# Kernel optimization log

Measured on AMD Instinct MI355X. Metric: run time of the kernel, lower is better.

## Reference

```python
import jax, jax.numpy as jnp
import numpy as np
import math

B, S, E = 4, 2048, 1024


def setup_inputs() -> dict:
    key = jax.random.key(0)
    ks = jax.random.split(key, 9)
    x = jax.random.normal(ks[0], (B, S, E), dtype=jnp.float32)
    # causal boolean mask, broadcast over batch: True = keep
    mask = jnp.broadcast_to(jnp.tril(jnp.ones((S, S), dtype=bool)), (B, S, S))
    sc = 1.0 / math.sqrt(E)
    Wq = jax.random.normal(ks[1], (E, E), dtype=jnp.float32) * sc
    bq = jnp.zeros((E,), dtype=jnp.float32)
    Wk = jax.random.normal(ks[2], (E, E), dtype=jnp.float32) * sc
    bk = jnp.zeros((E,), dtype=jnp.float32)
    Wv = jax.random.normal(ks[3], (E, E), dtype=jnp.float32) * sc
    bv = jnp.zeros((E,), dtype=jnp.float32)
    gamma = jnp.ones((E,), dtype=jnp.float32)
    beta = jnp.zeros((E,), dtype=jnp.float32)
    return {"x": x, "mask": mask, "Wq": Wq, "bq": bq, "Wk": Wk, "bk": bk,
            "Wv": Wv, "bv": bv, "gamma": gamma, "beta": beta}


def reference(x, mask, Wq, bq, Wk, bk, Wv, bv, gamma, beta):
    E_ = x.shape[-1]
    q = jnp.einsum('bse,fe->bsf', x, Wq) + bq
    k = jnp.einsum('bse,fe->bsf', x, Wk) + bk
    v = jnp.einsum('bse,fe->bsf', x, Wv) + bv
    scores = jnp.einsum('bqe,bke->bqk', q, k) / jnp.sqrt(jnp.float32(E_))
    scores = jnp.where(mask, scores, -jnp.inf)
    probs = jax.nn.softmax(scores, axis=-1)
    attn = jnp.einsum('bqk,bke->bqe', probs, v)
    y = attn + x
    # LayerNorm over last dim, eps matches torch default 1e-5
    mu = jnp.mean(y, axis=-1, keepdims=True)
    var = jnp.mean(jnp.square(y - mu), axis=-1, keepdims=True)
    return (y - mu) / jnp.sqrt(var + 1e-5) * gamma + beta
```

## Files before the change

### kernel.cpp

```cpp
#include <hip/hip_runtime.h>
#include <hip/hip_bf16.h>
#include <stdint.h>

#define B_ 4
#define S_ 2048
#define E_ 1024
#define BS_ (B_*S_)

using bf16x8 = __attribute__((ext_vector_type(8))) __bf16;
using f32x4  = __attribute__((ext_vector_type(4))) float;

__device__ __forceinline__ unsigned short f2bf(float f) {
  unsigned int u = __float_as_uint(f);
  u += 0x7fffu + ((u >> 16) & 1u);
  return (unsigned short)(u >> 16);
}
__device__ __forceinline__ float bf2f(unsigned short h) {
  return __uint_as_float(((unsigned int)h) << 16);
}

__device__ __forceinline__ void gld16(const unsigned short* g, unsigned short* l) {
  __builtin_amdgcn_global_load_lds((__attribute__((address_space(1))) void*)(void*)g,
                                   (__attribute__((address_space(3))) void*)l, 16, 0, 0);
}

__global__ __launch_bounds__(256) void conv_f32_bf16(const float* __restrict__ in,
                                                     unsigned short* __restrict__ out,
                                                     int n4) {
  int i = blockIdx.x * 256 + threadIdx.x;
  if (i >= n4) return;
  const float4 v = ((const float4*)in)[i];
  ushort4 o;
  o.x = f2bf(v.x); o.y = f2bf(v.y); o.z = f2bf(v.z); o.w = f2bf(v.w);
  ((ushort4*)out)[i] = o;
}

__global__ __launch_bounds__(256) void concat_bias(const float* __restrict__ a,
                                                   const float* __restrict__ b,
                                                   const float* __restrict__ c,
                                                   float* __restrict__ o) {
  int i = blockIdx.x * 256 + threadIdx.x;
  if (i >= 3 * E_) return;
  o[i] = (i < E_) ? a[i] : (i < 2 * E_ ? b[i - E_] : c[i - 2 * E_]);
}

template<int EPI>
__global__ __launch_bounds__(256, 2) void gemm_bt(
    const unsigned short* __restrict__ A, const unsigned short* __restrict__ Bm,
    float* __restrict__ Cf, unsigned short* __restrict__ Cb,
    const float* __restrict__ bias,
    int K, int lda, int ldb, int ldc,
    long sA, long sB, long sC, float scale, int causal)
{
  constexpr int BM = 128, BN = 128, BK = 64;
  __shared__ __align__(16) unsigned short As[BM * BK];
  __shared__ __align__(16) unsigned short Bs[BN * BK];
  const int bz = blockIdx.z;
  A  += sA * bz;
  Bm += sB * bz;
  const int m0 = blockIdx.y * BM, n0 = blockIdx.x * BN;
  if (EPI == 1 && causal && n0 >= m0 + BM) return;
  const int kend = (EPI == 2 && causal) ? min(K, m0 + BM) : K;
  const int t = threadIdx.x;
  const int lane = t & 63, wave = t >> 6;
  const int wr = wave >> 1, wc = wave & 1;
  const int q = lane >> 4, r = lane & 15;

  const int srow   = lane >> 3;
  const int schunk = (lane & 7) ^ srow;
  const long ga0 = (long)(m0 + wave * 32 + srow) * lda + schunk * 8;
  const long gb0 = (long)(n0 + wave * 32 + srow) * ldb + schunk * 8;

  f32x4 acc[4][4] = {};

  for (int k0 = 0; k0 < kend; k0 += BK) {
#pragma unroll
    for (int s = 0; s < 4; ++s) {
      gld16(A  + ga0 + (long)s * 8 * lda + k0, &As[(wave * 32 + s * 8) * 64]);
      gld16(Bm + gb0 + (long)s * 8 * ldb + k0, &Bs[(wave * 32 + s * 8) * 64]);
    }
    __syncthreads();
#pragma unroll
    for (int kk = 0; kk < BK; kk += 32) {
      bf16x8 af[4], bfr[4];
      const int cq = (kk >> 3) + q;
#pragma unroll
      for (int i = 0; i < 4; ++i) {
        const int row = wr * 64 + i * 16 + r;
        af[i] = *(const bf16x8*)&As[(row * 8 + (cq ^ (r & 7))) * 8];
      }
#pragma unroll
      for (int j = 0; j < 4; ++j) {
        const int row = wc * 64 + j * 16 + r;
        bfr[j] = *(const bf16x8*)&Bs[(row * 8 + (cq ^ (r & 7))) * 8];
      }
#pragma unroll
      for (int i = 0; i < 4; ++i)
#pragma unroll
        for (int j = 0; j < 4; ++j)
          acc[i][j] = __builtin_amdgcn_mfma_f32_16x16x32_bf16(af[i], bfr[j], acc[i][j], 0, 0, 0);
    }
    __syncthreads();
  }

  if (EPI == 2) Cf += sC * bz; else Cb += sC * bz;
#pragma unroll
  for (int i = 0; i < 4; ++i) {
#pragma unroll
    for (int j = 0; j < 4; ++j) {
      const int col = n0 + wc * 64 + j * 16 + r;
#pragma unroll
      for (int e = 0; e < 4; ++e) {
        const int rowg = m0 + wr * 64 + i * 16 + q * 4 + e;
        float v = acc[i][j][e];
        if (EPI == 0) {
          v += bias[col];
          Cb[(long)rowg * ldc + col] = f2bf(v);
        } else if (EPI == 1) {
          Cb[(long)rowg * ldc + col] = f2bf(v * scale);
        } else {
          Cf[(long)rowg * ldc + col] = v;
        }
      }
    }
  }
}

__global__ __launch_bounds__(256) void transpose_b(const unsigned short* __restrict__ V,
                                                   unsigned short* __restrict__ Vt, int lda) {
  __shared__ unsigned short tile[64][68];
  const int b = blockIdx.z;
  const unsigned short* Vb = V + (long)b * S_ * lda;
  unsigned short* Vtb = Vt + (long)b * S_ * E_;
  const int e0 = blockIdx.x * 64, j0 = blockIdx.y * 64;
  const int t = threadIdx.x;
#pragma unroll
  for (int i = 0; i < 4; ++i) {
    const int c = t + i * 256;
    const int row = c >> 4, c4 = c & 15;
    *(ushort4*)&tile[row][c4 * 4] = *(const ushort4*)&Vb[(long)(j0 + row) * lda + e0 + c4 * 4];
  }
  __syncthreads();
#pragma unroll
  for (int i = 0; i < 4; ++i) {
    const int c = t + i * 256;
    const int orow = c >> 4, c4 = c & 15;
    ushort4 o;
    o.x = tile[c4 * 4 + 0][orow];
    o.y = tile[c4 * 4 + 1][orow];
    o.z = tile[c4 * 4 + 2][orow];
    o.w = tile[c4 * 4 + 3][orow];
    *(ushort4*)&Vtb[(long)(e0 + orow) * S_ + j0 + c4 * 4] = o;
  }
}

__global__ __launch_bounds__(256) void softmax_causal(unsigned short* __restrict__ Sc) {
  const int row = blockIdx.x * 4 + (threadIdx.x >> 6);
  const int lane = threadIdx.x & 63;
  const int b = row >> 11, ii = row & (S_ - 1);
  unsigned short* prow = Sc + (long)b * S_ * S_ + (long)ii * S_;
  const int len = ii + 1;
  float v[32];
#pragma unroll
  for (int c = 0; c < 4; ++c) {
    const int base = (c * 64 + lane) * 8;
    if (base < len) {
      const uint4 u = *(const uint4*)&prow[base];
      const unsigned int w[4] = {u.x, u.y, u.z, u.w};
#pragma unroll
      for (int e = 0; e < 8; ++e) {
        const unsigned short h = (unsigned short)(w[e >> 1] >> ((e & 1) * 16));
        v[c * 8 + e] = (base + e < len) ? bf2f(h) : -3.0e38f;
      }
    } else {
#pragma unroll
      for (int e = 0; e < 8; ++e) v[c * 8 + e] = -3.0e38f;
    }
  }
  float mx = -3.0e38f;
#pragma unroll
  for (int i = 0; i < 32; ++i) mx = fmaxf(mx, v[i]);
#pragma unroll
  for (int o = 32; o; o >>= 1) mx = fmaxf(mx, __shfl_xor(mx, o));
  float sum = 0.f;
#pragma unroll
  for (int i = 0; i < 32; ++i) { v[i] = __expf(v[i] - mx); sum += v[i]; }
#pragma unroll
  for (int o = 32; o; o >>= 1) sum += __shfl_xor(sum, o);
  const float inv = 1.0f / sum;
#pragma unroll
  for (int c = 0; c < 4; ++c) {
    const int base = (c * 64 + lane) * 8;
    uint4 u;
    unsigned int w[4];
#pragma unroll
    for (int p = 0; p < 4; ++p) {
      const unsigned short lo = f2bf(v[c * 8 + p * 2] * inv);
      const unsigned short hi = f2bf(v[c * 8 + p * 2 + 1] * inv);
      w[p] = (unsigned int)lo | ((unsigned int)hi << 16);
    }
    u.x = w[0]; u.y = w[1]; u.z = w[2]; u.w = w[3];
    *(uint4*)&prow[base] = u;
  }
}

__global__ __launch_bounds__(256) void residual_ln(
    const float* __restrict__ attn, const float* __restrict__ x,
    const float* __restrict__ gamma, const float* __restrict__ beta,
    float* __restrict__ out) {
  __shared__ float rs[4], rs2[4];
  const long row = blockIdx.x;
  const int t = threadIdx.x;
  const int lane = t & 63, wave = t >> 6;
  const float4 a  = ((const float4*)(attn + row * E_))[t];
  const float4 xv = ((const float4*)(x + row * E_))[t];
  const float y0 = a.x + xv.x, y1 = a.y + xv.y, y2 = a.z + xv.z, y3 = a.w + xv.w;
  float s  = y0 + y1 + y2 + y3;
  float s2 = y0 * y0 + y1 * y1 + y2 * y2 + y3 * y3;
#pragma unroll
  for (int o = 32; o; o >>= 1) { s += __shfl_xor(s, o); s2 += __shfl_xor(s2, o); }
  if (lane == 0) { rs[wave] = s; rs2[wave] = s2; }
  __syncthreads();
  s  = rs[0] + rs[1] + rs[2] + rs[3];
  s2 = rs2[0] + rs2[1] + rs2[2] + rs2[3];
  const float mu  = s * (1.0f / E_);
  const float var = s2 * (1.0f / E_) - mu * mu;
  const float inv = rsqrtf(var + 1e-5f);
  const float4 g  = ((const float4*)gamma)[t];
  const float4 be = ((const float4*)beta)[t];
  float4 o;
  o.x = (y0 - mu) * inv * g.x + be.x;
  o.y = (y1 - mu) * inv * g.y + be.y;
  o.z = (y2 - mu) * inv * g.z + be.z;
  o.w = (y3 - mu) * inv * g.w + be.w;
  ((float4*)(out + row * E_))[t] = o;
}

extern "C" void kernel_launch(void* const* d_in, const int* in_sizes, int n_in,
                              void* d_out, int out_size, void* d_ws, size_t ws_size,
                              hipStream_t stream) {
  const float* x  = (const float*)d_in[0];
  const float* Wq = (const float*)d_in[2];
  const float* bq = (const float*)d_in[3];
  const float* Wk = (const float*)d_in[4];
  const float* bk = (const float*)d_in[5];
  const float* Wv = (const float*)d_in[6];
  const float* bv = (const float*)d_in[7];
  const float* gamma = (const float*)d_in[8];
  const float* beta  = (const float*)d_in[9];
  float* out = (float*)d_out;

  char* ws = (char*)d_ws;
  size_t off = 0;
  auto alloc = [&](size_t bytes) { char* p = ws + off; off += (bytes + 255) & ~(size_t)255; return p; };
  unsigned short* xb    = (unsigned short*)alloc((size_t)BS_ * E_ * 2);
  unsigned short* Wqkvb = (unsigned short*)alloc((size_t)3 * E_ * E_ * 2);
  float*          bqkv  = (float*)alloc((size_t)3 * E_ * 4);
  unsigned short* Cqkv  = (unsigned short*)alloc((size_t)BS_ * 3 * E_ * 2);
  unsigned short* Vt    = (unsigned short*)alloc((size_t)BS_ * E_ * 2);
  unsigned short* Sc    = (unsigned short*)alloc((size_t)B_ * S_ * S_ * 2);
  float* attn = (float*)Cqkv;

  conv_f32_bf16<<<dim3(BS_ * E_ / 4 / 256), 256, 0, stream>>>(x, xb, BS_ * E_ / 4);
  conv_f32_bf16<<<dim3(E_ * E_ / 4 / 256), 256, 0, stream>>>(Wq, Wqkvb, E_ * E_ / 4);
  conv_f32_bf16<<<dim3(E_ * E_ / 4 / 256), 256, 0, stream>>>(Wk, Wqkvb + E_ * E_, E_ * E_ / 4);
  conv_f32_bf16<<<dim3(E_ * E_ / 4 / 256), 256, 0, stream>>>(Wv, Wqkvb + 2 * E_ * E_, E_ * E_ / 4);
  concat_bias<<<dim3((3 * E_ + 255) / 256), 256, 0, stream>>>(bq, bk, bv, bqkv);

  dim3 g1(3 * E_ / 128, BS_ / 128, 1);
  gemm_bt<0><<<g1, 256, 0, stream>>>(xb, Wqkvb, nullptr, Cqkv, bqkv,
                                     E_, E_, E_, 3 * E_, 0, 0, 0, 1.f, 0);

  transpose_b<<<dim3(E_ / 64, S_ / 64, B_), 256, 0, stream>>>(Cqkv + 2 * E_, Vt, 3 * E_);

  dim3 g2(S_ / 128, S_ / 128, B_);
  gemm_bt<1><<<g2, 256, 0, stream>>>(Cqkv, Cqkv + E_, nullptr, Sc, nullptr,
                                     E_, 3 * E_, 3 * E_, S_,
                                     (long)S_ * 3 * E_, (long)S_ * 3 * E_, (long)S_ * S_,
                                     0.03125f, 1);

  softmax_causal<<<dim3(BS_ / 4), 256, 0, stream>>>(Sc);

  dim3 g3(E_ / 128, S_ / 128, B_);
  gemm_bt<2><<<g3, 256, 0, stream>>>(Sc, Vt, attn, nullptr, nullptr,
                                     S_, S_, S_, E_,
                                     (long)S_ * S_, (long)S_ * E_, (long)S_ * E_, 1.f, 1);

  residual_ln<<<dim3(BS_), 256, 0, stream>>>(attn, x, gamma, beta, out);
}
```

Measured before the change: 306.5 us.

## Fuse weight/bias prep kernels, raise GEMM occupancy, reverse causal tile order

Merges the three weight conversions and the bias concat into one launch, which removes kernel-launch overhead. Raises the GEMM launch-bounds occupancy hint from 2 to 3 blocks per CU, which can push register pressure and cause spills. For the causal score and PV GEMMs, the row-tile order is reversed so the heaviest tiles are dispatched first, which should give better load balance at the tail.

```diff
diff --git a/kernel.cpp b/kernel.cpp
--- a/kernel.cpp
+++ b/kernel.cpp
@@ -35,17 +35,27 @@
   ((ushort4*)out)[i] = o;
 }
 
-__global__ __launch_bounds__(256) void concat_bias(const float* __restrict__ a,
-                                                   const float* __restrict__ b,
-                                                   const float* __restrict__ c,
-                                                   float* __restrict__ o) {
-  int i = blockIdx.x * 256 + threadIdx.x;
-  if (i >= 3 * E_) return;
-  o[i] = (i < E_) ? a[i] : (i < 2 * E_ ? b[i - E_] : c[i - 2 * E_]);
+__global__ __launch_bounds__(256) void prep_w(
+    const float* __restrict__ Wq, const float* __restrict__ Wk, const float* __restrict__ Wv,
+    const float* __restrict__ bq, const float* __restrict__ bk, const float* __restrict__ bv,
+    unsigned short* __restrict__ Wb, float* __restrict__ bb) {
+  const int i = blockIdx.x * 256 + threadIdx.x;
+  const int n4 = E_ * E_ / 4;
+  if (i < 3 * n4) {
+    const int m = i / n4, j = i - m * n4;
+    const float* src = (m == 0) ? Wq : (m == 1) ? Wk : Wv;
+    const float4 v = ((const float4*)src)[j];
+    ushort4 o;
+    o.x = f2bf(v.x); o.y = f2bf(v.y); o.z = f2bf(v.z); o.w = f2bf(v.w);
+    ((ushort4*)Wb)[i] = o;
+  } else {
+    const int j = i - 3 * n4;
+    if (j < 3 * E_) bb[j] = (j < E_) ? bq[j] : (j < 2 * E_) ? bk[j - E_] : bv[j - 2 * E_];
+  }
 }
 
 template<int EPI>
-__global__ __launch_bounds__(256, 2) void gemm_bt(
+__global__ __launch_bounds__(256, 3) void gemm_bt(
     const unsigned short* __restrict__ A, const unsigned short* __restrict__ Bm,
     float* __restrict__ Cf, unsigned short* __restrict__ Cb,
     const float* __restrict__ bias,
@@ -58,7 +68,8 @@
   const int bz = blockIdx.z;
   A  += sA * bz;
   Bm += sB * bz;
-  const int m0 = blockIdx.y * BM, n0 = blockIdx.x * BN;
+  const int mt = (EPI != 0) ? (gridDim.y - 1 - blockIdx.y) : blockIdx.y;
+  const int m0 = mt * BM, n0 = blockIdx.x * BN;
   if (EPI == 1 && causal && n0 >= m0 + BM) return;
   const int kend = (EPI == 2 && causal) ? min(K, m0 + BM) : K;
   const int t = threadIdx.x;
@@ -262,10 +273,8 @@
   float* attn = (float*)Cqkv;
 
   conv_f32_bf16<<<dim3(BS_ * E_ / 4 / 256), 256, 0, stream>>>(x, xb, BS_ * E_ / 4);
-  conv_f32_bf16<<<dim3(E_ * E_ / 4 / 256), 256, 0, stream>>>(Wq, Wqkvb, E_ * E_ / 4);
-  conv_f32_bf16<<<dim3(E_ * E_ / 4 / 256), 256, 0, stream>>>(Wk, Wqkvb + E_ * E_, E_ * E_ / 4);
-  conv_f32_bf16<<<dim3(E_ * E_ / 4 / 256), 256, 0, stream>>>(Wv, Wqkvb + 2 * E_ * E_, E_ * E_ / 4);
-  concat_bias<<<dim3((3 * E_ + 255) / 256), 256, 0, stream>>>(bq, bk, bv, bqkv);
+  prep_w<<<dim3((3 * E_ * E_ / 4 + 3 * E_ + 255) / 256), 256, 0, stream>>>(
+      Wq, Wk, Wv, bq, bk, bv, Wqkvb, bqkv);
 
   dim3 g1(3 * E_ / 128, BS_ / 128, 1);
   gemm_bt<0><<<g1, 256, 0, stream>>>(xb, Wqkvb, nullptr, Cqkv, bqkv,
```

After: 307.3 us. No clear change (+0.3%).
